# Optimization experiments

Hardware: AMD Instinct MI355X
Metric: run time of the kernel (lower is better)

## Reference

```python
import jax, jax.numpy as jnp
import numpy as np

B, D, T = 16, 64, 3000
N_CB, K = 8, 1024


def setup_inputs() -> dict:
    key = jax.random.key(0)
    k1, k2 = jax.random.split(key)
    x = jax.random.normal(k1, (B, D, T), dtype=jnp.float32)
    embeds = jax.random.normal(k2, (N_CB, K, D), dtype=jnp.float32) * 0.02
    return {"x": x, "embeds": embeds}


def _vq_stage(r_flat, embed):
    """One VectorQuantize layer on flattened [N, D] input (eval mode).

    Returns (quantized_st [N,D], indices [N], commit+codebook loss, utilization).
    """
    # squared Euclidean distances [N, K]; argmin is identical to cdist argmin
    d2 = (jnp.sum(r_flat * r_flat, axis=-1, keepdims=True)
          - 2.0 * (r_flat @ embed.T)
          + jnp.sum(embed * embed, axis=-1))
    idx = jnp.argmin(d2, axis=-1)                      # [N]
    q = embed[idx]                                     # [N, D] gather
    sg = jax.lax.stop_gradient
    commit = jnp.mean((r_flat - sg(q)) ** 2)
    codebook = jnp.mean((q - sg(r_flat)) ** 2)
    q_st = r_flat + sg(q - r_flat)                     # straight-through
    used = jnp.zeros((K,), dtype=jnp.float32).at[idx].set(1.0)
    util = jnp.sum(used) / K                           # == len(unique)/K
    return q_st, idx, commit + codebook, util


def reference(x, embeds):
    """ResidualVQ forward (eval mode): x [B, D, T], embeds [n_cb, K, D]."""
    sg = jax.lax.stop_gradient
    residual = x
    quantized_total = jnp.zeros_like(x)
    all_indices = []
    total_commit = jnp.float32(0.0)
    total_util = jnp.float32(0.0)
    for i in range(N_CB):
        r_flat = residual.transpose(0, 2, 1).reshape(-1, D)  # [B*T, D]
        q_st_flat, idx, commit, util = _vq_stage(r_flat, embeds[i])
        q_st = q_st_flat.reshape(x.shape[0], x.shape[2], D).transpose(0, 2, 1)
        residual = residual - sg(q_st)
        quantized_total = quantized_total + q_st
        all_indices.append(idx)
        total_commit = total_commit + commit
        total_util = total_util + util
    indices = jnp.stack(all_indices, axis=0)           # [n_cb, B*T]
    return quantized_total, indices, total_commit / N_CB, total_util / N_CB
```

## Files before the change

kernel.cpp:

```cpp
#include <hip/hip_runtime.h>
#include <hip/hip_bf16.h>
#include <math.h>

#define Bn   16
#define Dn   64
#define Tn   3000
#define Nn   (Bn*Tn)
#define NCB  8
#define Kn   1024
#define KTB  64
#define NCHK (Kn/KTB)
#define NTB  64
#define NBLK (Nn/NTB)
#define EPSF 8e-3f
#define QMAX 512

#define SM_RH   0
#define SM_RL   8192
#define SM_EH   16384
#define SM_EL   24576
#define SM_RF   32768
#define SM_SE   49152
#define SM_SR   49408
#define SM_BEST 49664
#define SM_QCNT 50176
#define SM_QUE  50192
#define SM_BK   52240
#define SM_TOT  52496

#define WS_RES  0
#define WS_EHI  12288000
#define WS_ELO  13336576
#define WS_SE   14385152
#define WS_USED 14417920
#define WS_LOSS 14450688

#define OUT_QT_OFF  0
#define OUT_IDX_OFF 3072000
#define OUT_SC_OFF  3456000

typedef __attribute__((ext_vector_type(4))) float f32x4;
typedef __attribute__((ext_vector_type(8))) short s16x8;

__device__ __forceinline__ unsigned short f2bf(float x) {
    unsigned int u = __float_as_uint(x);
    unsigned int r = (u + 0x7FFFu + ((u >> 16) & 1u)) >> 16;
    return (unsigned short)r;
}
__device__ __forceinline__ float bf2f(unsigned short h) {
    return __uint_as_float(((unsigned int)h) << 16);
}

__global__ void vq_se(const float* __restrict__ emb, float* __restrict__ se)
{
    int r = blockIdx.x * 256 + threadIdx.x;
    if (r < NCB*Kn) {
        const float* p = emb + r*Dn;
        float a0=0.f, a1=0.f, a2=0.f, a3=0.f;
        #pragma unroll
        for (int d = 0; d < Dn; d += 4) {
            a0 = fmaf(p[d+0], p[d+0], a0);
            a1 = fmaf(p[d+1], p[d+1], a1);
            a2 = fmaf(p[d+2], p[d+2], a2);
            a3 = fmaf(p[d+3], p[d+3], a3);
        }
        se[r] = (a0+a1)+(a2+a3);
    }
}

__global__ void vq_ebf(const float* __restrict__ emb, char* __restrict__ ehi,
                       char* __restrict__ elo)
{
    int idx = blockIdx.x * 256 + threadIdx.x;
    int r = idx >> 3;
    int s = idx & 7;
    const float* p = emb + (size_t)r*Dn + s*8;
    s16x8 hh, ll;
    #pragma unroll
    for (int j = 0; j < 8; ++j) {
        float v = p[j];
        unsigned short h = f2bf(v);
        hh[j] = (short)h;
        ll[j] = (short)f2bf(v - bf2f(h));
    }
    int cb = r >> 10, kk = r & 1023, c = kk >> 6, kl = kk & 63;
    size_t off = (size_t)cb*131072 + (size_t)c*8192 + kl*128 + ((s ^ (kl & 7)) << 4);
    *(s16x8*)(ehi + off) = hh;
    *(s16x8*)(elo + off) = ll;
}

__device__ __forceinline__
float vq_rescore(const float* rf, float sr, float sek,
                 const float* __restrict__ emb_cb, int n, int kg)
{
    const float4* ep = (const float4*)(emb_cb + (size_t)kg*Dn);
    float q0=0.f,q1=0.f,q2=0.f,q3=0.f;
    #pragma unroll 4
    for (int m = 0; m < 16; ++m) {
        float4 e4 = ep[m];
        q0 = fmaf(rf[(4*m+0)*64 + n], e4.x, q0);
        q1 = fmaf(rf[(4*m+1)*64 + n], e4.y, q1);
        q2 = fmaf(rf[(4*m+2)*64 + n], e4.z, q2);
        q3 = fmaf(rf[(4*m+3)*64 + n], e4.w, q3);
    }
    float dot = (q0+q1)+(q2+q3);
    return (sr - 2.0f*dot) + sek;
}

__global__ __launch_bounds__(256, 3)
void vq_mega(const float* __restrict__ x, const float* __restrict__ emb,
             const char* __restrict__ ehib, const char* __restrict__ elob,
             const float* __restrict__ se_g,
             float* __restrict__ out_qt, float* __restrict__ out_idx,
             float* __restrict__ used_g, float* __restrict__ loss_acc)
{
    __shared__ __align__(16) char smem[SM_TOT];
    float*  rf     = (float*)(smem + SM_RF);
    float*  selds  = (float*)(smem + SM_SE);
    float*  lds_sr = (float*)(smem + SM_SR);
    unsigned long long* best64 = (unsigned long long*)(smem + SM_BEST);
    int*    qcnt   = (int*)(smem + SM_QCNT);
    unsigned int* que = (unsigned int*)(smem + SM_QUE);
    float*  srpart = (float*)(smem + SM_QUE);
    int*    bkL    = (int*)(smem + SM_BK);

    const int tid = threadIdx.x;
    const int n0 = blockIdx.x * NTB;
    const int lane = tid & 63, w = tid >> 6;
    const int lrow = lane & 15, lhi = lane >> 4;
    const int nl = tid & 63;
    const int dg = tid >> 6;
    const float4* hsrc = (const float4*)ehib;
    const float4* lsrc = (const float4*)elob;

    {
        const int n = n0 + nl;
        const int b = n / Tn, t = n % Tn;
        const float* gp = x + b*(Dn*Tn) + t;
        float v[16];
        #pragma unroll
        for (int j = 0; j < 16; ++j) v[j] = gp[(dg*16 + j)*Tn];
        float a0=0.f,a1=0.f,a2=0.f,a3=0.f;
        #pragma unroll
        for (int j = 0; j < 16; j += 4) {
            a0 = fmaf(v[j+0], v[j+0], a0);
            a1 = fmaf(v[j+1], v[j+1], a1);
            a2 = fmaf(v[j+2], v[j+2], a2);
            a3 = fmaf(v[j+3], v[j+3], a3);
        }
        srpart[dg*64 + nl] = (a0+a1)+(a2+a3);
        unsigned short hi[16], lo[16];
        #pragma unroll
        for (int j = 0; j < 16; ++j) {
            rf[(dg*16 + j)*64 + nl] = v[j];
            hi[j] = f2bf(v[j]);
            lo[j] = f2bf(v[j] - bf2f(hi[j]));
        }
        s16x8 ph0, ph1, pl0, pl1;
        #pragma unroll
        for (int j = 0; j < 8; ++j) {
            ph0[j] = (short)hi[j];   ph1[j] = (short)hi[j+8];
            pl0[j] = (short)lo[j];   pl1[j] = (short)lo[j+8];
        }
        const int s0 = dg*2, s1 = dg*2 + 1, nx = nl & 7;
        *(s16x8*)(smem + SM_RH + nl*128 + ((s0 ^ nx) << 4)) = ph0;
        *(s16x8*)(smem + SM_RH + nl*128 + ((s1 ^ nx) << 4)) = ph1;
        *(s16x8*)(smem + SM_RL + nl*128 + ((s0 ^ nx) << 4)) = pl0;
        *(s16x8*)(smem + SM_RL + nl*128 + ((s1 ^ nx) << 4)) = pl1;
    }
    if (tid < 64) best64[tid] = ~0ULL;
    if (tid == 0) qcnt[0] = 0;
    __syncthreads();
    if (tid < 64)
        lds_sr[tid] = (srpart[tid] + srpart[64+tid]) + (srpart[128+tid] + srpart[192+tid]);
    ((float4*)(smem + SM_EH))[tid]      = hsrc[tid];
    ((float4*)(smem + SM_EH))[tid+256]  = hsrc[tid+256];
    ((float4*)(smem + SM_EL))[tid]      = lsrc[tid];
    ((float4*)(smem + SM_EL))[tid+256]  = lsrc[tid+256];
    if (tid < 64) selds[tid] = se_g[tid];

    float lsum = 0.f;

    for (int s = 0; s < NCB; ++s) {
        const float* emb_s = emb + (size_t)s*(Kn*Dn);
        float m_run = INFINITY;

        for (int c = 0; c < NCHK; ++c) {
            __syncthreads();
            const bool pre = (c < NCHK-1) || (s < NCB-1);
            float4 h0, h1, l0, l1; float sepre = 0.f;
            if (pre) {
                size_t nb = (c < NCHK-1) ? ((size_t)s*8192 + (size_t)(c+1)*512)
                                         : ((size_t)(s+1)*8192);
                h0 = hsrc[nb + tid]; h1 = hsrc[nb + 256 + tid];
                l0 = lsrc[nb + tid]; l1 = lsrc[nb + 256 + tid];
                if (tid < 64)
                    sepre = se_g[(c < NCHK-1) ? (s*Kn + (c+1)*KTB + tid)
                                              : ((s+1)*Kn + tid)];
            }

            f32x4 acc[4] = {};
            #pragma unroll
            for (int ks = 0; ks < 2; ++ks) {
                const int sdim = ks*4 + lhi;
                const int swz = ((sdim ^ (lrow & 7)) << 4);
                const size_t roff = (size_t)(w*16 + lrow)*128 + swz;
                const size_t eoff = (size_t)lrow*128 + swz;
                s16x8 bh = *(const s16x8*)(smem + SM_RH + roff);
                s16x8 bl = *(const s16x8*)(smem + SM_RL + roff);
                #pragma unroll
                for (int i = 0; i < 4; ++i) {
                    s16x8 ah = *(const s16x8*)(smem + SM_EH + eoff + i*2048);
                    s16x8 al = *(const s16x8*)(smem + SM_EL + eoff + i*2048);
                    acc[i] = __builtin_amdgcn_mfma_f32_16x16x32_bf16(ah, bh, acc[i], 0, 0, 0);
                    acc[i] = __builtin_amdgcn_mfma_f32_16x16x32_bf16(ah, bl, acc[i], 0, 0, 0);
                    acc[i] = __builtin_amdgcn_mfma_f32_16x16x32_bf16(al, bh, acc[i], 0, 0, 0);
                }
            }

            float cv[4][4];
            float m = INFINITY;
            #pragma unroll
            for (int i = 0; i < 4; ++i)
                #pragma unroll
                for (int rg = 0; rg < 4; ++rg) {
                    float c2 = selds[i*16 + lhi*4 + rg] - 2.0f*acc[i][rg];
                    cv[i][rg] = c2;
                    m = fminf(m, c2);
                }
            m = fminf(m, __shfl_xor(m, 16, 64));
            m = fminf(m, __shfl_xor(m, 32, 64));
            const float thr = fminf(m_run, m) + EPSF;
            m_run = fminf(m_run, m);
            const int nlocal = w*16 + lrow;

            #pragma unroll
            for (int i = 0; i < 4; ++i)
                #pragma unroll
                for (int rg = 0; rg < 4; ++rg) {
                    if (cv[i][rg] <= thr) {
                        int kl = i*16 + lhi*4 + rg;
                        int kg = c*KTB + kl;
                        int slot = atomicAdd(qcnt, 1);
                        if (slot < QMAX) {
                            que[slot] = ((unsigned)nlocal << 10) | (unsigned)kg;
                        } else {
                            float d2e = vq_rescore(rf, lds_sr[nlocal], selds[kl],
                                                   emb_s, nlocal, kg);
                            unsigned long long pk =
                                ((unsigned long long)__float_as_uint(d2e) << 32) | (unsigned)kg;
                            atomicMin(&best64[nlocal], pk);
                        }
                    }
                }
            __syncthreads();
            if (pre) {
                ((float4*)(smem + SM_EH))[tid]     = h0;
                ((float4*)(smem + SM_EH))[tid+256] = h1;
                ((float4*)(smem + SM_EL))[tid]     = l0;
                ((float4*)(smem + SM_EL))[tid+256] = l1;
                if (tid < 64) selds[tid] = sepre;
            }
        }

        const int cnt = min(qcnt[0], QMAX);
        for (int e = tid; e < cnt; e += 256) {
            unsigned ent = que[e];
            int nn = (int)(ent >> 10);
            int kg = (int)(ent & 1023);
            float sek = se_g[s*Kn + kg];
            float d2e = vq_rescore(rf, lds_sr[nn], sek, emb_s, nn, kg);
            unsigned long long pk =
                ((unsigned long long)__float_as_uint(d2e) << 32) | (unsigned)kg;
            atomicMin(&best64[nn], pk);
        }
        __syncthreads();

        if (tid < 64) {
            int bk = (int)(best64[tid] & 0xFFFFFFFFull) & (Kn - 1);
            bkL[tid] = bk;
            out_idx[s*Nn + n0 + tid] = (float)bk;
            used_g[s*Kn + bk] = 1.0f;
            best64[tid] = ~0ULL;
        }
        if (tid == 0) qcnt[0] = 0;
        __syncthreads();

        const float* ep = emb_s + (size_t)bkL[nl]*Dn;
        if (s < NCB-1) {
            float nv[16];
            #pragma unroll
            for (int j = 0; j < 16; ++j) {
                int d = dg*16 + j;
                float rv = rf[d*64 + nl];
                float q  = ep[d];
                float diff = rv - q;
                lsum = fmaf(diff, diff, lsum);
                float qst = rv + (q - rv);
                nv[j] = rv - qst;
                rf[d*64 + nl] = nv[j];
            }
            float a0=0.f,a1=0.f,a2=0.f,a3=0.f;
            #pragma unroll
            for (int j = 0; j < 16; j += 4) {
                a0 = fmaf(nv[j+0], nv[j+0], a0);
                a1 = fmaf(nv[j+1], nv[j+1], a1);
                a2 = fmaf(nv[j+2], nv[j+2], a2);
                a3 = fmaf(nv[j+3], nv[j+3], a3);
            }
            srpart[dg*64 + nl] = (a0+a1)+(a2+a3);
            unsigned short hi[16], lo[16];
            #pragma unroll
            for (int j = 0; j < 16; ++j) {
                hi[j] = f2bf(nv[j]);
                lo[j] = f2bf(nv[j] - bf2f(hi[j]));
            }
            s16x8 ph0, ph1, pl0, pl1;
            #pragma unroll
            for (int j = 0; j < 8; ++j) {
                ph0[j] = (short)hi[j];   ph1[j] = (short)hi[j+8];
                pl0[j] = (short)lo[j];   pl1[j] = (short)lo[j+8];
            }
            const int s0 = dg*2, s1 = dg*2 + 1, nx = nl & 7;
            *(s16x8*)(smem + SM_RH + nl*128 + ((s0 ^ nx) << 4)) = ph0;
            *(s16x8*)(smem + SM_RH + nl*128 + ((s1 ^ nx) << 4)) = ph1;
            *(s16x8*)(smem + SM_RL + nl*128 + ((s0 ^ nx) << 4)) = pl0;
            *(s16x8*)(smem + SM_RL + nl*128 + ((s1 ^ nx) << 4)) = pl1;
            __syncthreads();
            if (tid < 64)
                lds_sr[tid] = (srpart[tid] + srpart[64+tid])
                            + (srpart[128+tid] + srpart[192+tid]);
        } else {
            const int n = n0 + nl;
            const int b = n / Tn, t = n % Tn;
            const float* xp = x + b*(Dn*Tn) + t;
            float* qp = out_qt + b*(Dn*Tn) + t;
            #pragma unroll
            for (int j = 0; j < 16; ++j) {
                int d = dg*16 + j;
                float rv = rf[d*64 + nl];
                float q  = ep[d];
                float diff = rv - q;
                lsum = fmaf(diff, diff, lsum);
                float qst = rv + (q - rv);
                float rn = rv - qst;
                qp[d*Tn] = xp[d*Tn] - rn;
            }
        }
    }

    float* red = (float*)(smem + SM_QUE);
    red[tid] = lsum;
    __syncthreads();
    for (int s2 = 128; s2 > 0; s2 >>= 1) {
        if (tid < s2) red[tid] += red[tid + s2];
        __syncthreads();
    }
    if (tid == 0) atomicAdd(loss_acc, red[0]);
}

__global__ void vq_scalars(const float* __restrict__ used, const float* __restrict__ loss_acc,
                           float* __restrict__ out)
{
    __shared__ float red[256];
    float s = 0.f;
    for (int j = threadIdx.x; j < NCB*Kn; j += 256) s += used[j];
    red[threadIdx.x] = s;
    __syncthreads();
    for (int st = 128; st > 0; st >>= 1) {
        if (threadIdx.x < st) red[threadIdx.x] += red[threadIdx.x + st];
        __syncthreads();
    }
    if (threadIdx.x == 0) {
        float sumsq = loss_acc[0];
        float total_loss = 2.0f * sumsq / (float)(Nn*Dn);
        out[OUT_SC_OFF + 0] = total_loss / (float)NCB;
        out[OUT_SC_OFF + 1] = red[0] / (float)(NCB*Kn);
    }
}

extern "C" void kernel_launch(void* const* d_in, const int* in_sizes, int n_in,
                              void* d_out, int out_size, void* d_ws, size_t ws_size,
                              hipStream_t stream)
{
    const float* x      = (const float*)d_in[0];
    const float* embeds = (const float*)d_in[1];
    float* out = (float*)d_out;
    char* ws = (char*)d_ws;

    char*  ehi  = ws + WS_EHI;
    char*  elo  = ws + WS_ELO;
    float* se   = (float*)(ws + WS_SE);
    float* used = (float*)(ws + WS_USED);
    float* loss = (float*)(ws + WS_LOSS);

    hipMemsetAsync(used, 0, (size_t)NCB*Kn*sizeof(float) + 16, stream);

    vq_se<<<(NCB*Kn + 255)/256, 256, 0, stream>>>(embeds, se);
    vq_ebf<<<256, 256, 0, stream>>>(embeds, ehi, elo);

    vq_mega<<<NBLK, 256, 0, stream>>>(x, embeds, ehi, elo, se,
                                      out + OUT_QT_OFF, out + OUT_IDX_OFF,
                                      used, loss);

    vq_scalars<<<1, 256, 0, stream>>>(used, loss, out);
}
```

Baseline: 337.2 us.

## Drop embedding low-part MFMA and use per-row adaptive rescoring band

Removes the bf16 low half of the codebook, so each chunk runs two MFMAs instead of three, and stops loading or storing the low-part buffer. Exactness now relies on a per-row error band computed from the row norm and the largest codebook norm, with candidates inside the band rescored in fp32. The K chunk grows to 128 codes, which halves the number of chunk iterations and barriers. Candidate scanning is gated per 16-code group by a wave-level any(). This risks a larger candidate queue and fallback rescoring when the band is wide.

```diff
diff --git a/kernel.cpp b/kernel.cpp
--- a/kernel.cpp
+++ b/kernel.cpp
@@ -8,32 +8,29 @@
 #define Nn   (Bn*Tn)
 #define NCB  8
 #define Kn   1024
-#define KTB  64
+#define KTB  128
 #define NCHK (Kn/KTB)
 #define NTB  64
 #define NBLK (Nn/NTB)
-#define EPSF 8e-3f
-#define QMAX 512
+#define QMAX 768
 
 #define SM_RH   0
 #define SM_RL   8192
 #define SM_EH   16384
-#define SM_EL   24576
 #define SM_RF   32768
 #define SM_SE   49152
-#define SM_SR   49408
-#define SM_BEST 49664
-#define SM_QCNT 50176
-#define SM_QUE  50192
-#define SM_BK   52240
-#define SM_TOT  52496
-
-#define WS_RES  0
-#define WS_EHI  12288000
-#define WS_ELO  13336576
-#define WS_SE   14385152
-#define WS_USED 14417920
-#define WS_LOSS 14450688
+#define SM_SR   49664
+#define SM_BEST 49920
+#define SM_QCNT 50432
+#define SM_QUE  50448
+#define SM_BK   53520
+#define SM_TOT  53776
+
+#define WS_EHI   12288000
+#define WS_SE    13336576
+#define WS_USED  13369344
+#define WS_LOSS  13402112
+#define WS_SEMAX 13402128
 
 #define OUT_QT_OFF  0
 #define OUT_IDX_OFF 3072000
@@ -51,7 +48,8 @@
     return __uint_as_float(((unsigned int)h) << 16);
 }
 
-__global__ void vq_se(const float* __restrict__ emb, float* __restrict__ se)
+__global__ void vq_se(const float* __restrict__ emb, float* __restrict__ se,
+                      float* __restrict__ semax)
 {
     int r = blockIdx.x * 256 + threadIdx.x;
     if (r < NCB*Kn) {
@@ -64,29 +62,24 @@
             a2 = fmaf(p[d+2], p[d+2], a2);
             a3 = fmaf(p[d+3], p[d+3], a3);
         }
-        se[r] = (a0+a1)+(a2+a3);
-    }
-}
-
-__global__ void vq_ebf(const float* __restrict__ emb, char* __restrict__ ehi,
-                       char* __restrict__ elo)
+        float v = (a0+a1)+(a2+a3);
+        se[r] = v;
+        atomicMax((int*)&semax[r >> 10], __float_as_int(v));
+    }
+}
+
+__global__ void vq_ebf(const float* __restrict__ emb, char* __restrict__ ehi)
 {
     int idx = blockIdx.x * 256 + threadIdx.x;
     int r = idx >> 3;
     int s = idx & 7;
     const float* p = emb + (size_t)r*Dn + s*8;
-    s16x8 hh, ll;
+    s16x8 hh;
     #pragma unroll
-    for (int j = 0; j < 8; ++j) {
-        float v = p[j];
-        unsigned short h = f2bf(v);
-        hh[j] = (short)h;
-        ll[j] = (short)f2bf(v - bf2f(h));
-    }
-    int cb = r >> 10, kk = r & 1023, c = kk >> 6, kl = kk & 63;
-    size_t off = (size_t)cb*131072 + (size_t)c*8192 + kl*128 + ((s ^ (kl & 7)) << 4);
+    for (int j = 0; j < 8; ++j) hh[j] = (short)f2bf(p[j]);
+    int cb = r >> 10, kk = r & 1023, c = kk >> 7, kl = kk & 127;
+    size_t off = (size_t)cb*131072 + (size_t)c*16384 + (size_t)kl*128 + ((s ^ (kl & 7)) << 4);
     *(s16x8*)(ehi + off) = hh;
-    *(s16x8*)(elo + off) = ll;
 }
 
 __device__ __forceinline__
@@ -109,8 +102,8 @@
 
 __global__ __launch_bounds__(256, 3)
 void vq_mega(const float* __restrict__ x, const float* __restrict__ emb,
-             const char* __restrict__ ehib, const char* __restrict__ elob,
-             const float* __restrict__ se_g,
+             const char* __restrict__ ehib, const float* __restrict__ se_g,
+             const float* __restrict__ semax_g,
              float* __restrict__ out_qt, float* __restrict__ out_idx,
              float* __restrict__ used_g, float* __restrict__ loss_acc)
 {
@@ -131,7 +124,6 @@
     const int nl = tid & 63;
     const int dg = tid >> 6;
     const float4* hsrc = (const float4*)ehib;
-    const float4* lsrc = (const float4*)elob;
 
     {
         const int n = n0 + nl;
@@ -173,33 +165,41 @@
     __syncthreads();
     if (tid < 64)
         lds_sr[tid] = (srpart[tid] + srpart[64+tid]) + (srpart[128+tid] + srpart[192+tid]);
-    ((float4*)(smem + SM_EH))[tid]      = hsrc[tid];
-    ((float4*)(smem + SM_EH))[tid+256]  = hsrc[tid+256];
-    ((float4*)(smem + SM_EL))[tid]      = lsrc[tid];
-    ((float4*)(smem + SM_EL))[tid+256]  = lsrc[tid+256];
-    if (tid < 64) selds[tid] = se_g[tid];
+    ((float4*)(smem + SM_EH))[tid]       = hsrc[tid];
+    ((float4*)(smem + SM_EH))[tid+256]   = hsrc[tid+256];
+    ((float4*)(smem + SM_EH))[tid+512]   = hsrc[tid+512];
+    ((float4*)(smem + SM_EH))[tid+768]   = hsrc[tid+768];
+    if (tid < KTB) selds[tid] = se_g[tid];
 
     float lsum = 0.f;
+    const int nlocal = w*16 + lrow;
 
     for (int s = 0; s < NCB; ++s) {
         const float* emb_s = emb + (size_t)s*(Kn*Dn);
+        const float semx = semax_g[s];
         float m_run = INFINITY;
+        float band = 0.f;
 
         for (int c = 0; c < NCHK; ++c) {
             __syncthreads();
+            if (c == 0)
+                band = 0.0095f * sqrtf(semx * lds_sr[nlocal]) + 2e-4f;
+
             const bool pre = (c < NCHK-1) || (s < NCB-1);
-            float4 h0, h1, l0, l1; float sepre = 0.f;
+            float4 h0, h1, h2, h3; float sepre = 0.f;
             if (pre) {
-                size_t nb = (c < NCHK-1) ? ((size_t)s*8192 + (size_t)(c+1)*512)
+                size_t nb = (c < NCHK-1) ? ((size_t)s*8192 + (size_t)(c+1)*1024)
                                          : ((size_t)(s+1)*8192);
-                h0 = hsrc[nb + tid]; h1 = hsrc[nb + 256 + tid];
-                l0 = lsrc[nb + tid]; l1 = lsrc[nb + 256 + tid];
-                if (tid < 64)
+                h0 = hsrc[nb + tid];       h1 = hsrc[nb + 256 + tid];
+                h2 = hsrc[nb + 512 + tid]; h3 = hsrc[nb + 768 + tid];
+                if (tid < KTB)
                     sepre = se_g[(c < NCHK-1) ? (s*Kn + (c+1)*KTB + tid)
                                               : ((s+1)*Kn + tid)];
             }
 
-            f32x4 acc[4] = {};
+            f32x4 acc[8];
+            #pragma unroll
+            for (int i = 0; i < 8; ++i) acc[i] = (f32x4){0.f,0.f,0.f,0.f};
             #pragma unroll
             for (int ks = 0; ks < 2; ++ks) {
                 const int sdim = ks*4 + lhi;
@@ -209,57 +209,58 @@
                 s16x8 bh = *(const s16x8*)(smem + SM_RH + roff);
                 s16x8 bl = *(const s16x8*)(smem + SM_RL + roff);
                 #pragma unroll
-                for (int i = 0; i < 4; ++i) {
+                for (int i = 0; i < 8; ++i) {
                     s16x8 ah = *(const s16x8*)(smem + SM_EH + eoff + i*2048);
-                    s16x8 al = *(const s16x8*)(smem + SM_EL + eoff + i*2048);
                     acc[i] = __builtin_amdgcn_mfma_f32_16x16x32_bf16(ah, bh, acc[i], 0, 0, 0);
                     acc[i] = __builtin_amdgcn_mfma_f32_16x16x32_bf16(ah, bl, acc[i], 0, 0, 0);
-                    acc[i] = __builtin_amdgcn_mfma_f32_16x16x32_bf16(al, bh, acc[i], 0, 0, 0);
                 }
             }
 
-            float cv[4][4];
+            float mi[8];
             float m = INFINITY;
             #pragma unroll
-            for (int i = 0; i < 4; ++i)
+            for (int i = 0; i < 8; ++i) {
                 #pragma unroll
-                for (int rg = 0; rg < 4; ++rg) {
-                    float c2 = selds[i*16 + lhi*4 + rg] - 2.0f*acc[i][rg];
-                    cv[i][rg] = c2;
-                    m = fminf(m, c2);
-                }
+                for (int rg = 0; rg < 4; ++rg)
+                    acc[i][rg] = selds[i*16 + lhi*4 + rg] - 2.0f*acc[i][rg];
+                float a = fminf(fminf(acc[i][0], acc[i][1]), fminf(acc[i][2], acc[i][3]));
+                mi[i] = a;
+                m = fminf(m, a);
+            }
             m = fminf(m, __shfl_xor(m, 16, 64));
             m = fminf(m, __shfl_xor(m, 32, 64));
-            const float thr = fminf(m_run, m) + EPSF;
+            const float thr = fminf(m_run, m) + band;
             m_run = fminf(m_run, m);
-            const int nlocal = w*16 + lrow;
-
-            #pragma unroll
-            for (int i = 0; i < 4; ++i)
-                #pragma unroll
-                for (int rg = 0; rg < 4; ++rg) {
-                    if (cv[i][rg] <= thr) {
-                        int kl = i*16 + lhi*4 + rg;
-                        int kg = c*KTB + kl;
-                        int slot = atomicAdd(qcnt, 1);
-                        if (slot < QMAX) {
-                            que[slot] = ((unsigned)nlocal << 10) | (unsigned)kg;
-                        } else {
-                            float d2e = vq_rescore(rf, lds_sr[nlocal], selds[kl],
-                                                   emb_s, nlocal, kg);
-                            unsigned long long pk =
-                                ((unsigned long long)__float_as_uint(d2e) << 32) | (unsigned)kg;
-                            atomicMin(&best64[nlocal], pk);
+
+            #pragma unroll
+            for (int i = 0; i < 8; ++i) {
+                if (__any(mi[i] <= thr)) {
+                    #pragma unroll
+                    for (int rg = 0; rg < 4; ++rg) {
+                        if (acc[i][rg] <= thr) {
+                            int kl = i*16 + lhi*4 + rg;
+                            int kg = c*KTB + kl;
+                            int slot = atomicAdd(qcnt, 1);
+                            if (slot < QMAX) {
+                                que[slot] = ((unsigned)nlocal << 10) | (unsigned)kg;
+                            } else {
+                                float d2e = vq_rescore(rf, lds_sr[nlocal], selds[kl],
+                                                       emb_s, nlocal, kg);
+                                unsigned long long pk =
+                                    ((unsigned long long)__float_as_uint(d2e) << 32) | (unsigned)kg;
+                                atomicMin(&best64[nlocal], pk);
+                            }
                         }
                     }
                 }
+            }
             __syncthreads();
             if (pre) {
                 ((float4*)(smem + SM_EH))[tid]     = h0;
                 ((float4*)(smem + SM_EH))[tid+256] = h1;
-                ((float4*)(smem + SM_EL))[tid]     = l0;
-                ((float4*)(smem + SM_EL))[tid+256] = l1;
-                if (tid < 64) selds[tid] = sepre;
+                ((float4*)(smem + SM_EH))[tid+512] = h2;
+                ((float4*)(smem + SM_EH))[tid+768] = h3;
+                if (tid < KTB) selds[tid] = sepre;
             }
         }
 
@@ -388,18 +389,18 @@
     float* out = (float*)d_out;
     char* ws = (char*)d_ws;
 
-    char*  ehi  = ws + WS_EHI;
-    char*  elo  = ws + WS_ELO;
-    float* se   = (float*)(ws + WS_SE);
-    float* used = (float*)(ws + WS_USED);
-    float* loss = (float*)(ws + WS_LOSS);
-
-    hipMemsetAsync(used, 0, (size_t)NCB*Kn*sizeof(float) + 16, stream);
-
-    vq_se<<<(NCB*Kn + 255)/256, 256, 0, stream>>>(embeds, se);
-    vq_ebf<<<256, 256, 0, stream>>>(embeds, ehi, elo);
-
-    vq_mega<<<NBLK, 256, 0, stream>>>(x, embeds, ehi, elo, se,
+    char*  ehi   = ws + WS_EHI;
+    float* se    = (float*)(ws + WS_SE);
+    float* used  = (float*)(ws + WS_USED);
+    float* loss  = (float*)(ws + WS_LOSS);
+    float* semax = (float*)(ws + WS_SEMAX);
+
+    hipMemsetAsync(used, 0, (size_t)NCB*Kn*sizeof(float) + 48, stream);
+
+    vq_se<<<(NCB*Kn + 255)/256, 256, 0, stream>>>(embeds, se, semax);
+    vq_ebf<<<256, 256, 0, stream>>>(embeds, ehi);
+
+    vq_mega<<<NBLK, 256, 0, stream>>>(x, embeds, ehi, se, semax,
                                       out + OUT_QT_OFF, out + OUT_IDX_OFF,
                                       used, loss);
 
```

Measured after the change: 692.7 us. 105% more time.
